# Kernel optimization log

Measured on AMD Instinct MI355X. Metric: run time of the kernel, lower is better.

Reference implementation:

```python
import jax, jax.numpy as jnp
import numpy as np

N_HEADS, D, D_HEAD = 16, 1024, 64
B, T = 4, 2048


def setup_inputs() -> dict:
    key = jax.random.key(0)
    k1, k2, k3, k4, k5, k6, k7 = jax.random.split(key, 7)
    Q = jax.random.normal(k1, (B, T, D), dtype=jnp.float32)
    K = jax.random.normal(k2, (B, T, D), dtype=jnp.float32)
    V = jax.random.normal(k3, (B, T, D), dtype=jnp.float32)
    # params initialized as 0.001 * randn, matching create_head
    Wq = 0.001 * jax.random.normal(k4, (N_HEADS, D, D_HEAD), dtype=jnp.float32)
    Wk = 0.001 * jax.random.normal(k5, (N_HEADS, D, D_HEAD), dtype=jnp.float32)
    Wv = 0.001 * jax.random.normal(k6, (N_HEADS, D, D_HEAD), dtype=jnp.float32)
    Wo = 0.001 * jax.random.normal(k7, (N_HEADS * D_HEAD, D), dtype=jnp.float32)
    return {"Q": Q, "K": K, "V": V, "Wq": Wq, "Wk": Wk, "Wv": Wv, "Wo": Wo}


def reference(Q, K, V, Wq, Wk, Wv, Wo):
    # per-head projections: [b,t,d] x [h,d,e] -> [b,h,t,e]
    Qh = jnp.einsum('btd,hde->bhte', Q, Wq)
    Kh = jnp.einsum('btd,hde->bhte', K, Wk)
    Vh = jnp.einsum('btd,hde->bhte', V, Wv)
    # scaled dot-product attention (ar=False path)
    scale = 1.0 / jnp.sqrt(jnp.asarray(D_HEAD, Qh.dtype))
    s = jnp.einsum('bhqe,bhke->bhqk', Qh, Kh) * scale  # [b,h,t,t]
    s = jax.nn.softmax(s, axis=-1)
    attn = jnp.einsum('bhqk,bhke->bhqe', s, Vh)  # [b,h,t,e]
    # output projection: rearrange b h t e -> b (h e) t, then 'bht,hd->btd'
    # equivalent to contracting (h,e) against Wo reshaped to [h,e,D]
    Wo3 = Wo.reshape(N_HEADS, D_HEAD, D)
    out = jnp.einsum('bhte,heD->btD', attn, Wo3)  # [b,t,d]
    return out
```

## Files before the change

### kernel.cpp

```cpp
#include <hip/hip_runtime.h>
#include <hip/hip_bf16.h>

#define DEV __device__ __forceinline__

typedef __attribute__((ext_vector_type(8))) short short8;
typedef __attribute__((ext_vector_type(4))) float f32x4;
typedef __attribute__((ext_vector_type(16))) float f32x16;
typedef __attribute__((ext_vector_type(2))) unsigned int u32x2;
typedef __attribute__((ext_vector_type(4))) unsigned int u32x4;
typedef unsigned short u16;
typedef unsigned int u32;


DEV u16 f2bf(float f) {
    union { __hip_bfloat16 h; u16 u; } cv;
    cv.h = __float2bfloat16(f);
    return cv.u;
}

DEV float exp2_raw(float x) {
    float r;
    asm("v_exp_f32 %0, %1" : "=v"(r) : "v"(x));
    return r;
}

DEV u32 cvtpk_bf2(float lo, float hi) {
    u32 r;
    asm("v_cvt_pk_bf16_f32 %0, %1, %2" : "=v"(r) : "v"(lo), "v"(hi));
    return r;
}

DEV void gload_lds16(const void* g, void* l) {
    __builtin_amdgcn_global_load_lds((const __attribute__((address_space(1))) u32*)g,
                                     (__attribute__((address_space(3))) u32*)l, 16, 0, 0);
}

__global__ __launch_bounds__(256) void k_transpose_w3(const float* __restrict__ W0,
                                                      const float* __restrict__ W1,
                                                      const float* __restrict__ W2,
                                                      u16* __restrict__ O0,
                                                      u16* __restrict__ O1,
                                                      u16* __restrict__ O2) {
    __shared__ float tile[64][65];
    const int x = threadIdx.x & 63, y = threadIdx.x >> 6;
    const int which = blockIdx.z >> 4, slab_i = blockIdx.z & 15;
    const float* in = which == 0 ? W0 : (which == 1 ? W1 : W2);
    u16* out = which == 0 ? O0 : (which == 1 ? O1 : O2);
    const float sc = which == 0 ? 0.18033688011112042f : 1.0f;
    const long slab = (long)slab_i * 1024 * 64;
    const int r0 = blockIdx.x * 64;
#pragma unroll
    for (int i = 0; i < 16; ++i) {
        int rr = y + 4 * i;
        tile[rr][x] = in[slab + (long)(r0 + rr) * 64 + x];
    }
    __syncthreads();
#pragma unroll
    for (int i = 0; i < 16; ++i) {
        int cc = y + 4 * i;
        out[slab + (long)cc * 1024 + (r0 + x)] = f2bf(tile[x][cc] * sc);
    }
}

__global__ __launch_bounds__(256) void k_transpose_f32_bf16(const float* __restrict__ in,
                                                            u16* __restrict__ out,
                                                            int R, int C) {
    __shared__ float tile[64][65];
    const int x = threadIdx.x & 63, y = threadIdx.x >> 6;
    const long slab = (long)blockIdx.z * R * C;
    const int r0 = blockIdx.x * 64, c0 = blockIdx.y * 64;
#pragma unroll
    for (int i = 0; i < 16; ++i) {
        int rr = y + 4 * i;
        tile[rr][x] = in[slab + (long)(r0 + rr) * C + (c0 + x)];
    }
    __syncthreads();
#pragma unroll
    for (int i = 0; i < 16; ++i) {
        int cc = y + 4 * i;
        out[slab + (long)(c0 + cc) * R + (r0 + x)] = f2bf(tile[x][cc]);
    }
}

__global__ __launch_bounds__(512, 4) void k_gemm3(const float* __restrict__ Aq, const float* __restrict__ Ak,
                                                  const float* __restrict__ Av,
                                                  const u16* __restrict__ B0, const u16* __restrict__ B1,
                                                  const u16* __restrict__ B2,
                                                  u16* __restrict__ C0, u16* __restrict__ C1,
                                                  u16* __restrict__ C2) {
    __shared__ u16 As[2 * 8192];
    __shared__ u16 Bs[2 * 8192];
    const int tid = threadIdx.x, lane = tid & 63, w = tid >> 6;
    const int l15 = lane & 15, l4 = lane >> 4;
    const int wr = w >> 2, wc = w & 3;
    const int hw = blockIdx.x;
    const int lg = (hw & 7) * 192 + (hw >> 3);
    const int z = lg >> 9, rem = lg & 511;
    const int brow = (rem >> 3) * 128, bcol = (rem & 7) * 128;
    const float* Af = z == 0 ? Aq : (z == 1 ? Ak : Av);
    const u16*   Bt = z == 0 ? B0 : (z == 1 ? B1 : B2);
    u16*         Cb = z == 0 ? C0 : (z == 1 ? C1 : C2);

    const float* aptr[2]; int adst[2];
#pragma unroll
    for (int i = 0; i < 2; ++i) {
        const int c = i * 512 + tid;
        const int r = c >> 3, s = c & 7;
        aptr[i] = Af + (long)(brow + r) * 1024 + s * 8;
        adst[i] = r * 64 + (s ^ (r & 7)) * 8;
    }
    const u16* bptr[2]; int bdst[2];
#pragma unroll
    for (int i = 0; i < 2; ++i) {
        const int c = i * 512 + w * 64 + lane;
        const int r = c >> 3, s = c & 7, sw = s ^ (r & 7);
        bptr[i] = Bt + (long)(bcol + r) * 1024 + sw * 8;
        bdst[i] = i * 4096 + w * 512;
    }

    int e4[2];
#pragma unroll
    for (int kk = 0; kk < 2; ++kk) e4[kk] = ((kk * 4 + l4) ^ (l15 & 7)) * 8;
    int offA[4][2], offB[2][2];
#pragma unroll
    for (int kk = 0; kk < 2; ++kk) {
#pragma unroll
        for (int m = 0; m < 4; ++m)
            offA[m][kk] = (wr * 64 + m * 16 + l15) * 64 + e4[kk];
#pragma unroll
        for (int n = 0; n < 2; ++n)
            offB[n][kk] = (wc * 32 + n * 16 + l15) * 64 + e4[kk];
    }

    f32x4 acc[4][2] = {};
    float4 va0[2][2], va1[2][2];

#define ISSUE_A(SET, kt) do { _Pragma("unroll") for (int i = 0; i < 2; ++i) {          \
        va##SET[i][0] = *(const float4*)(aptr[i] + (kt) * 64);                          \
        va##SET[i][1] = *(const float4*)(aptr[i] + (kt) * 64 + 4); } } while (0)
#define ISSUE_B(buf, kt) do {                                                           \
        gload_lds16(bptr[0] + (kt) * 64, Bs + (buf) * 8192 + bdst[0]);                  \
        gload_lds16(bptr[1] + (kt) * 64, Bs + (buf) * 8192 + bdst[1]); } while (0)

    ISSUE_A(0, 0); ISSUE_B(0, 0);
    ISSUE_A(1, 1); ISSUE_B(1, 1);

#define GITER(t, SET) do {                                                              \
    if ((t) < 15) asm volatile("s_waitcnt vmcnt(6)" ::: "memory");                      \
    else          asm volatile("s_waitcnt vmcnt(0)" ::: "memory");                      \
    __builtin_amdgcn_sched_barrier(0);                                                  \
    { u16* Ad = As + ((t) & 1) * 8192;                                                  \
      _Pragma("unroll") for (int i = 0; i < 2; ++i) {                                   \
        u32x4 wv;                                                                       \
        wv[0] = cvtpk_bf2(va##SET[i][0].x, va##SET[i][0].y);                            \
        wv[1] = cvtpk_bf2(va##SET[i][0].z, va##SET[i][0].w);                            \
        wv[2] = cvtpk_bf2(va##SET[i][1].x, va##SET[i][1].y);                            \
        wv[3] = cvtpk_bf2(va##SET[i][1].z, va##SET[i][1].w);                            \
        *(u32x4*)&Ad[adst[i]] = wv; } }                                                 \
    asm volatile("s_waitcnt lgkmcnt(0)" ::: "memory");                                  \
    __builtin_amdgcn_sched_barrier(0);                                                  \
    __builtin_amdgcn_s_barrier();                                                       \
    __builtin_amdgcn_sched_barrier(0);                                                  \
    { const u16* Ab = As + ((t) & 1) * 8192;                                            \
      const u16* Bb = Bs + ((t) & 1) * 8192;                                            \
      _Pragma("unroll") for (int kk = 0; kk < 2; ++kk) {                                \
        short8 af[4], bfv[2];                                                           \
        _Pragma("unroll") for (int m = 0; m < 4; ++m) af[m] = *(const short8*)&Ab[offA[m][kk]]; \
        _Pragma("unroll") for (int n = 0; n < 2; ++n) bfv[n] = *(const short8*)&Bb[offB[n][kk]]; \
        asm volatile("s_waitcnt lgkmcnt(0)" ::: "memory");                              \
        __builtin_amdgcn_sched_barrier(0);                                              \
        __builtin_amdgcn_s_setprio(1);                                                  \
        _Pragma("unroll") for (int m = 0; m < 4; ++m)                                   \
        _Pragma("unroll") for (int n = 0; n < 2; ++n)                                   \
            acc[m][n] = __builtin_amdgcn_mfma_f32_16x16x32_bf16(af[m], bfv[n], acc[m][n], 0, 0, 0); \
        __builtin_amdgcn_s_setprio(0);                                                  \
        __builtin_amdgcn_sched_barrier(0); } }                                          \
    __builtin_amdgcn_s_barrier();                                                       \
    __builtin_amdgcn_sched_barrier(0);                                                  \
    if ((t) + 2 < 16) { ISSUE_A(SET, (t) + 2); ISSUE_B((t) & 1, (t) + 2); }             \
} while (0)

    for (int th = 0; th < 8; ++th) {
        GITER(2 * th, 0);
        GITER(2 * th + 1, 1);
    }
#undef GITER
#undef ISSUE_A
#undef ISSUE_B

    if (z == 2) {
#pragma unroll
        for (int m = 0; m < 4; ++m)
#pragma unroll
            for (int n = 0; n < 2; ++n) {
                const int tb = brow + wr * 64 + m * 16 + l4 * 4;
                const int ncol = bcol + wc * 32 + n * 16 + l15;
                const int b = tb >> 11, tt = tb & 2047;
                const int h = ncol >> 6, e = ncol & 63;
                u32x2 st;
                st[0] = cvtpk_bf2(acc[m][n][0], acc[m][n][1]);
                st[1] = cvtpk_bf2(acc[m][n][2], acc[m][n][3]);
                *(u32x2*)(Cb + (long)(b * 16 + h) * 131072 + (long)e * 2048 + tt) = st;
            }
    } else {
#pragma unroll
        for (int m = 0; m < 4; ++m)
#pragma unroll
            for (int n = 0; n < 2; ++n)
#pragma unroll
                for (int r = 0; r < 4; ++r) {
                    const long row = brow + wr * 64 + m * 16 + l4 * 4 + r;
                    const int col = bcol + wc * 32 + n * 16 + l15;
                    Cb[row * 1024 + col] = f2bf(acc[m][n][r]);
                }
    }
}

__global__ __launch_bounds__(512, 4) void k_gemm_out(const u16* __restrict__ Ap,
                                                     const u16* __restrict__ Bt,
                                                     float* __restrict__ Cf) {
    __shared__ u16 As[2 * 8192];
    __shared__ u16 Bs[2 * 8192];
    const int tid = threadIdx.x, lane = tid & 63, w = tid >> 6;
    const int l15 = lane & 15, l4 = lane >> 4;
    const int wr = w >> 2, wc = w & 3;
    const int hw = blockIdx.x;
    const int lg = (hw & 7) * 64 + (hw >> 3);
    const int brow = (lg >> 3) * 128, bcol = (lg & 7) * 128;

    const u16* aptr[2]; int adst[2];
#pragma unroll
    for (int i = 0; i < 2; ++i) {
        const int c = i * 512 + w * 64 + lane;
        const int r = c >> 3, s = c & 7, sw = s ^ (r & 7);
        aptr[i] = Ap + (long)(brow + r) * 1024 + sw * 8;
        adst[i] = i * 4096 + w * 512;
    }
    const u16* bptr[2]; int bdst[2];
#pragma unroll
    for (int i = 0; i < 2; ++i) {
        const int c = i * 512 + w * 64 + lane;
        const int r = c >> 3, s = c & 7, sw = s ^ (r & 7);
        bptr[i] = Bt + (long)(bcol + r) * 1024 + sw * 8;
        bdst[i] = i * 4096 + w * 512;
    }

    auto stage = [&](int buf, int kt) {
        const int ko = kt * 64;
        u16* Ad = As + buf * 8192;
        u16* Bd = Bs + buf * 8192;
#pragma unroll
        for (int i = 0; i < 2; ++i) gload_lds16(aptr[i] + ko, Ad + adst[i]);
#pragma unroll
        for (int i = 0; i < 2; ++i) gload_lds16(bptr[i] + ko, Bd + bdst[i]);
    };

    int e4[2];
#pragma unroll
    for (int kk = 0; kk < 2; ++kk) e4[kk] = ((kk * 4 + l4) ^ (l15 & 7)) * 8;
    int offA[4][2], offB[2][2];
#pragma unroll
    for (int kk = 0; kk < 2; ++kk) {
#pragma unroll
        for (int m = 0; m < 4; ++m)
            offA[m][kk] = (wr * 64 + m * 16 + l15) * 64 + e4[kk];
#pragma unroll
        for (int n = 0; n < 2; ++n)
            offB[n][kk] = (wc * 32 + n * 16 + l15) * 64 + e4[kk];
    }

    f32x4 acc[4][2] = {};
    stage(0, 0);
    stage(1, 1);

    for (int t = 0; t < 16; ++t) {
        const int buf = t & 1;
        if (t < 15) asm volatile("s_waitcnt vmcnt(4)" ::: "memory");
        else        asm volatile("s_waitcnt vmcnt(0)" ::: "memory");
        __builtin_amdgcn_sched_barrier(0);
        __builtin_amdgcn_s_barrier();
        __builtin_amdgcn_sched_barrier(0);

        const u16* Ab = As + buf * 8192;
        const u16* Bb = Bs + buf * 8192;
#pragma unroll
        for (int kk = 0; kk < 2; ++kk) {
            short8 af[4], bfv[2];
#pragma unroll
            for (int m = 0; m < 4; ++m) af[m] = *(const short8*)&Ab[offA[m][kk]];
#pragma unroll
            for (int n = 0; n < 2; ++n) bfv[n] = *(const short8*)&Bb[offB[n][kk]];
            asm volatile("s_waitcnt lgkmcnt(0)" ::: "memory");
            __builtin_amdgcn_sched_barrier(0);
            __builtin_amdgcn_s_setprio(1);
#pragma unroll
            for (int m = 0; m < 4; ++m)
#pragma unroll
                for (int n = 0; n < 2; ++n)
                    acc[m][n] = __builtin_amdgcn_mfma_f32_16x16x32_bf16(af[m], bfv[n], acc[m][n], 0, 0, 0);
            __builtin_amdgcn_s_setprio(0);
            __builtin_amdgcn_sched_barrier(0);
        }
        __builtin_amdgcn_s_barrier();
        __builtin_amdgcn_sched_barrier(0);
        if (t + 2 < 16) stage(buf, t + 2);
    }

#pragma unroll
    for (int m = 0; m < 4; ++m)
#pragma unroll
        for (int n = 0; n < 2; ++n)
#pragma unroll
            for (int r = 0; r < 4; ++r) {
                const long row = brow + wr * 64 + m * 16 + l4 * 4 + r;
                const int col = bcol + wc * 32 + n * 16 + l15;
                Cf[row * 1024 + col] = acc[m][n][r];
            }
}

__global__ __launch_bounds__(256, 2) void k_flash8(const u16* __restrict__ Qp,
                                                   const u16* __restrict__ Kp,
                                                   const u16* __restrict__ VhT,
                                                   u16* __restrict__ attn) {
    __shared__ u16 Ks[2][4096];
    __shared__ u16 Vs[2][4096];

    const int tid = threadIdx.x, lane = tid & 63, w = tid >> 6;
    const int l31 = lane & 31, l5 = lane >> 5;
    const int wid = blockIdx.x;
    const int swz = (wid & 7) * 64 + (wid >> 3);
    const int bh = swz >> 3, qt = swz & 7;
    const int b = bh >> 4, h = bh & 15;
    const long rowb = (long)b * 2048;
    const int colb = h * 64;
    const u16* Kbase = Kp + rowb * 1024 + colb;
    const long vbase = (long)bh * 131072;
    const int q0 = qt * 256 + w * 64;

    short8 qf0[4], qf1[4];
#pragma unroll
    for (int ksd = 0; ksd < 4; ++ksd) {
        qf0[ksd] = *(const short8*)(Qp + (rowb + q0 + l31) * 1024 + colb + ksd * 16 + l5 * 8);
        qf1[ksd] = *(const short8*)(Qp + (rowb + q0 + 32 + l31) * 1024 + colb + ksd * 16 + l5 * 8);
    }

    int off[4];
#pragma unroll
    for (int ksd = 0; ksd < 4; ++ksd)
        off[ksd] = l31 * 128 + (((ksd * 2 + l5) ^ (l31 & 7)) << 4);

    const float OFFS = 0.0625f;
    float lr0 = 0.f, lr1 = 0.f;
    f32x16 oa00 = {}, oa01 = {}, oa10 = {}, oa11 = {};

    const int c0 = tid, c1 = tid + 256;
    const int r0 = c0 >> 3, s0 = (c0 & 7) ^ (r0 & 7);
    const int r1 = c1 >> 3, s1 = (c1 & 7) ^ (r1 & 7);

#define STAGE(buf, t) do {                                                               \
    const long kv0_ = (long)((t) * 64);                                                  \
    gload_lds16(Kbase + (kv0_ + r0) * 1024 + s0 * 8, &Ks[buf][w * 512]);                 \
    gload_lds16(Kbase + (kv0_ + r1) * 1024 + s1 * 8, &Ks[buf][2048 + w * 512]);          \
    gload_lds16(VhT + vbase + (long)r0 * 2048 + kv0_ + s0 * 8, &Vs[buf][w * 512]);       \
    gload_lds16(VhT + vbase + (long)r1 * 2048 + kv0_ + s1 * 8, &Vs[buf][2048 + w * 512]); \
  } while (0)

    auto process_half = [&](const f32x16& zz, float& lr, short8* pb2) {
        u32 W[8];
        float rs = 0.f;
#pragma unroll
        for (int mw = 0; mw < 8; ++mw) {
            const float p0 = exp2_raw(zz[2 * mw] - OFFS);
            const float p1 = exp2_raw(zz[2 * mw + 1] - OFFS);
            rs += p0 + p1;
            W[mw] = cvtpk_bf2(p0, p1);
        }
        lr += rs;
#pragma unroll
        for (int ksw = 0; ksw < 2; ++ksw) {
            u32x2 ra = __builtin_amdgcn_permlane32_swap(W[4 * ksw + 0], W[4 * ksw + 2], false, false);
            u32x2 rb = __builtin_amdgcn_permlane32_swap(W[4 * ksw + 1], W[4 * ksw + 3], false, false);
            u32x4 pw; pw[0] = ra[0]; pw[1] = rb[0]; pw[2] = ra[1]; pw[3] = rb[1];
            pb2[ksw] = __builtin_bit_cast(short8, pw);
        }
    };

    STAGE(0, 0);
    STAGE(1, 1);

    for (int t = 0; t < 32; ++t) {
        const int buf = t & 1;
        if (t < 31) asm volatile("s_waitcnt vmcnt(4)" ::: "memory");
        else        asm volatile("s_waitcnt vmcnt(0)" ::: "memory");
        __builtin_amdgcn_sched_barrier(0);
        __builtin_amdgcn_s_barrier();
        __builtin_amdgcn_sched_barrier(0);

        const char* Kb = (const char*)&Ks[buf][0];
        const char* Vb = (const char*)&Vs[buf][0];

#pragma unroll
        for (int kvh = 0; kvh < 2; ++kvh) {
            short8 kf[4];
#pragma unroll
            for (int ksd = 0; ksd < 4; ++ksd)
                kf[ksd] = *(const short8*)(Kb + kvh * 4096 + off[ksd]);
            f32x16 z0 = {}, z1 = {};
            __builtin_amdgcn_s_setprio(1);
#pragma unroll
            for (int ksd = 0; ksd < 4; ++ksd) {
                z0 = __builtin_amdgcn_mfma_f32_32x32x16_bf16(kf[ksd], qf0[ksd], z0, 0, 0, 0);
                z1 = __builtin_amdgcn_mfma_f32_32x32x16_bf16(kf[ksd], qf1[ksd], z1, 0, 0, 0);
            }
            __builtin_amdgcn_s_setprio(0);

            short8 pb0[2], pb1[2];
            process_half(z0, lr0, pb0);
            process_half(z1, lr1, pb1);

            __builtin_amdgcn_s_setprio(1);
#pragma unroll
            for (int ksw = 0; ksw < 2; ++ksw) {
                const int ks = kvh * 2 + ksw;
                short8 vf0 = *(const short8*)(Vb + off[ks]);
                short8 vf1 = *(const short8*)(Vb + 4096 + off[ks]);
                oa00 = __builtin_amdgcn_mfma_f32_32x32x16_bf16(vf0, pb0[ksw], oa00, 0, 0, 0);
                oa01 = __builtin_amdgcn_mfma_f32_32x32x16_bf16(vf1, pb0[ksw], oa01, 0, 0, 0);
                oa10 = __builtin_amdgcn_mfma_f32_32x32x16_bf16(vf0, pb1[ksw], oa10, 0, 0, 0);
                oa11 = __builtin_amdgcn_mfma_f32_32x32x16_bf16(vf1, pb1[ksw], oa11, 0, 0, 0);
            }
            __builtin_amdgcn_s_setprio(0);
        }

        __builtin_amdgcn_s_barrier();
        __builtin_amdgcn_sched_barrier(0);
        if (t + 2 < 32) STAGE(buf, t + 2);
    }
#undef STAGE

    {
        u32x2 p0 = __builtin_amdgcn_permlane32_swap(__builtin_bit_cast(u32, lr0),
                                                    __builtin_bit_cast(u32, lr0), false, false);
        lr0 = __builtin_bit_cast(float, p0[0]) + __builtin_bit_cast(float, p0[1]);
        u32x2 p1 = __builtin_amdgcn_permlane32_swap(__builtin_bit_cast(u32, lr1),
                                                    __builtin_bit_cast(u32, lr1), false, false);
        lr1 = __builtin_bit_cast(float, p1[0]) + __builtin_bit_cast(float, p1[1]);
    }

#pragma unroll
    for (int g = 0; g < 2; ++g) {
        const float inv = 1.0f / (g ? lr1 : lr0);
        u16* op = attn + (rowb + q0 + g * 32 + l31) * 1024 + colb;
#pragma unroll
        for (int et = 0; et < 2; ++et) {
            const f32x16& oa = g ? (et ? oa11 : oa10) : (et ? oa01 : oa00);
#pragma unroll
            for (int rq = 0; rq < 4; ++rq) {
                u32x2 st;
                st[0] = cvtpk_bf2(oa[4 * rq + 0] * inv, oa[4 * rq + 1] * inv);
                st[1] = cvtpk_bf2(oa[4 * rq + 2] * inv, oa[4 * rq + 3] * inv);
                *(u32x2*)(op + et * 32 + rq * 8 + l5 * 4) = st;
            }
        }
    }
}

extern "C" void kernel_launch(void* const* d_in, const int* in_sizes, int n_in,
                              void* d_out, int out_size, void* d_ws, size_t ws_size,
                              hipStream_t stream) {
    (void)in_sizes; (void)n_in; (void)out_size; (void)ws_size;
    const float* Q  = (const float*)d_in[0];
    const float* K  = (const float*)d_in[1];
    const float* V  = (const float*)d_in[2];
    const float* Wq = (const float*)d_in[3];
    const float* Wk = (const float*)d_in[4];
    const float* Wv = (const float*)d_in[5];
    const float* Wo = (const float*)d_in[6];

    char* ws = (char*)d_ws;
    auto WS = [&](size_t mb) { return (u16*)(ws + (mb << 20)); };
    u16* WqT  = WS(0);
    u16* WkT  = WS(2);
    u16* WvT  = WS(4);
    u16* WoT  = WS(6);
    u16* Qp   = WS(8);
    u16* Kp   = WS(24);
    u16* VhT  = WS(40);
    u16* attn = WS(56);

    dim3 b256(256);
    dim3 b512(512);
    k_transpose_w3<<<dim3(16, 1, 48), b256, 0, stream>>>(Wq, Wk, Wv, WqT, WkT, WvT);
    k_transpose_f32_bf16<<<dim3(16, 16, 1), b256, 0, stream>>>(Wo, WoT, 1024, 1024);

    k_gemm3<<<dim3(1536), b512, 0, stream>>>(Q, K, V, WqT, WkT, WvT, Qp, Kp, VhT);

    k_flash8<<<dim3(512), b256, 0, stream>>>(Qp, Kp, VhT, attn);

    k_gemm_out<<<dim3(512), b512, 0, stream>>>(attn, WoT, (float*)d_out);
}
```

Before: 185.3 us.

## Deepen projection GEMM pipeline to three A register sets with deferred conversion

Restructures the projection GEMM main loop so the fp32 A operand is prefetched three k-tiles ahead into three register sets. The bf16 conversion and LDS store of the next A tile now happen after the current tile's MFMA compute instead of before it, and waitcnt thresholds are adjusted per iteration. The loop is fully unrolled by hand. This is meant to hide global load latency better and take the conversion off the critical path, at the cost of more VGPRs, which may reduce occupancy.

```diff
diff --git a/kernel.cpp b/kernel.cpp
--- a/kernel.cpp
+++ b/kernel.cpp
@@ -133,37 +133,35 @@
     }
 
     f32x4 acc[4][2] = {};
-    float4 va0[2][2], va1[2][2];
+    float4 va0[2][2], va1[2][2], va2[2][2];
 
 #define ISSUE_A(SET, kt) do { _Pragma("unroll") for (int i = 0; i < 2; ++i) {          \
         va##SET[i][0] = *(const float4*)(aptr[i] + (kt) * 64);                          \
         va##SET[i][1] = *(const float4*)(aptr[i] + (kt) * 64 + 4); } } while (0)
-#define ISSUE_B(buf, kt) do {                                                           \
-        gload_lds16(bptr[0] + (kt) * 64, Bs + (buf) * 8192 + bdst[0]);                  \
-        gload_lds16(bptr[1] + (kt) * 64, Bs + (buf) * 8192 + bdst[1]); } while (0)
-
-    ISSUE_A(0, 0); ISSUE_B(0, 0);
-    ISSUE_A(1, 1); ISSUE_B(1, 1);
-
-#define GITER(t, SET) do {                                                              \
-    if ((t) < 15) asm volatile("s_waitcnt vmcnt(6)" ::: "memory");                      \
-    else          asm volatile("s_waitcnt vmcnt(0)" ::: "memory");                      \
-    __builtin_amdgcn_sched_barrier(0);                                                  \
-    { u16* Ad = As + ((t) & 1) * 8192;                                                  \
+#define ISSUE_B(kt) do {                                                                \
+        gload_lds16(bptr[0] + (kt) * 64, Bs + ((kt) & 1) * 8192 + bdst[0]);             \
+        gload_lds16(bptr[1] + (kt) * 64, Bs + ((kt) & 1) * 8192 + bdst[1]); } while (0)
+#define CVT_A(SET, kt) do { u16* Ad = As + ((kt) & 1) * 8192;                           \
       _Pragma("unroll") for (int i = 0; i < 2; ++i) {                                   \
         u32x4 wv;                                                                       \
         wv[0] = cvtpk_bf2(va##SET[i][0].x, va##SET[i][0].y);                            \
         wv[1] = cvtpk_bf2(va##SET[i][0].z, va##SET[i][0].w);                            \
         wv[2] = cvtpk_bf2(va##SET[i][1].x, va##SET[i][1].y);                            \
         wv[3] = cvtpk_bf2(va##SET[i][1].z, va##SET[i][1].w);                            \
-        *(u32x4*)&Ad[adst[i]] = wv; } }                                                 \
-    asm volatile("s_waitcnt lgkmcnt(0)" ::: "memory");                                  \
-    __builtin_amdgcn_sched_barrier(0);                                                  \
-    __builtin_amdgcn_s_barrier();                                                       \
-    __builtin_amdgcn_sched_barrier(0);                                                  \
-    { const u16* Ab = As + ((t) & 1) * 8192;                                            \
-      const u16* Bb = Bs + ((t) & 1) * 8192;                                            \
-      _Pragma("unroll") for (int kk = 0; kk < 2; ++kk) {                                \
+        *(u32x4*)&Ad[adst[i]] = wv; } } while (0)
+
+    ISSUE_B(0); ISSUE_A(0, 0);
+    ISSUE_A(1, 1);
+    ISSUE_B(1);
+    ISSUE_A(2, 2);
+    asm volatile("s_waitcnt vmcnt(10)" ::: "memory");
+    __builtin_amdgcn_sched_barrier(0);
+    CVT_A(0, 0);
+
+#define COMPUTE(T) do {                                                                 \
+    const u16* Ab = As + ((T) & 1) * 8192;                                              \
+    const u16* Bb = Bs + ((T) & 1) * 8192;                                              \
+    _Pragma("unroll") for (int kk = 0; kk < 2; ++kk) {                                  \
         short8 af[4], bfv[2];                                                           \
         _Pragma("unroll") for (int m = 0; m < 4; ++m) af[m] = *(const short8*)&Ab[offA[m][kk]]; \
         _Pragma("unroll") for (int n = 0; n < 2; ++n) bfv[n] = *(const short8*)&Bb[offB[n][kk]]; \
@@ -174,19 +172,47 @@
         _Pragma("unroll") for (int n = 0; n < 2; ++n)                                   \
             acc[m][n] = __builtin_amdgcn_mfma_f32_16x16x32_bf16(af[m], bfv[n], acc[m][n], 0, 0, 0); \
         __builtin_amdgcn_s_setprio(0);                                                  \
-        __builtin_amdgcn_sched_barrier(0); } }                                          \
+        __builtin_amdgcn_sched_barrier(0); }                                            \
+} while (0)
+
+#define GITER(T, CV, IS, W1, W2, DOB, DOA) do {                                         \
+    asm volatile("s_waitcnt vmcnt(" #W1 ") lgkmcnt(0)" ::: "memory");                   \
+    __builtin_amdgcn_sched_barrier(0);                                                  \
     __builtin_amdgcn_s_barrier();                                                       \
     __builtin_amdgcn_sched_barrier(0);                                                  \
-    if ((t) + 2 < 16) { ISSUE_A(SET, (t) + 2); ISSUE_B((t) & 1, (t) + 2); }             \
+    COMPUTE(T);                                                                         \
+    __builtin_amdgcn_s_barrier();                                                       \
+    __builtin_amdgcn_sched_barrier(0);                                                  \
+    if ((T) < 15) {                                                                     \
+        asm volatile("s_waitcnt vmcnt(" #W2 ")" ::: "memory");                          \
+        __builtin_amdgcn_sched_barrier(0);                                              \
+        CVT_A(CV, (T) + 1);                                                             \
+    }                                                                                   \
+    if (DOB) ISSUE_B((T) + 2);                                                          \
+    if (DOA) ISSUE_A(IS, (T) + 3);                                                      \
 } while (0)
 
-    for (int th = 0; th < 8; ++th) {
-        GITER(2 * th, 0);
-        GITER(2 * th + 1, 1);
-    }
+    GITER(0,  1, 0, 10, 6, 1, 1);
+    GITER(1,  2, 1, 10, 6, 1, 1);
+    GITER(2,  0, 2, 10, 6, 1, 1);
+    GITER(3,  1, 0, 10, 6, 1, 1);
+    GITER(4,  2, 1, 10, 6, 1, 1);
+    GITER(5,  0, 2, 10, 6, 1, 1);
+    GITER(6,  1, 0, 10, 6, 1, 1);
+    GITER(7,  2, 1, 10, 6, 1, 1);
+    GITER(8,  0, 2, 10, 6, 1, 1);
+    GITER(9,  1, 0, 10, 6, 1, 1);
+    GITER(10, 2, 1, 10, 6, 1, 1);
+    GITER(11, 0, 2, 10, 6, 1, 1);
+    GITER(12, 1, 0, 10, 6, 1, 1);
+    GITER(13, 2, 0, 10, 6, 1, 0);
+    GITER(14, 0, 0, 6,  2, 0, 0);
+    GITER(15, 0, 0, 0,  0, 0, 0);
 #undef GITER
+#undef COMPUTE
+#undef CVT_A
+#undef ISSUE_B
 #undef ISSUE_A
-#undef ISSUE_B
 
     if (z == 2) {
 #pragma unroll
```

Result: slower. 190.3 us (+2.7%).
